# Kernel tuning notes

Measured on AMD Instinct MI355X. Metric: run time of the kernel, lower is better.

## Reference

```python
import jax, jax.numpy as jnp
import numpy as np

EPS = 1e-3  # Keras BatchNormalization default epsilon


def _bn(x, gamma, beta, mean, var):
    # inference-mode batchnorm over channel axis (last)
    inv = gamma * jax.lax.rsqrt(var + EPS)
    return x * inv + (beta - mean * inv)


def setup_inputs() -> dict:
    key = jax.random.key(0)
    ks = jax.random.split(key, 12)
    B, H, W, Cin = 8, 128, 128, 256
    F = 128  # f_g == f_l
    inp = {
        "input_g": jax.random.normal(ks[0], (B, H, W, Cin), jnp.float32),
        "input_x": jax.random.normal(ks[1], (B, H, W, Cin), jnp.float32),
        # w_g branch: 1x1 conv (channel GEMM) + BN
        "Wg": jax.random.normal(ks[2], (Cin, F), jnp.float32) * 0.05,
        "bg": jnp.zeros((F,), jnp.float32),
        "gamma_g": jax.random.uniform(ks[3], (F,), jnp.float32, 0.5, 1.5),
        "beta_g": jax.random.normal(ks[4], (F,), jnp.float32) * 0.1,
        "mean_g": jax.random.normal(ks[5], (F,), jnp.float32) * 0.1,
        "var_g": jax.random.uniform(ks[6], (F,), jnp.float32, 0.5, 1.5),
        # w_x branch
        "Wx": jax.random.normal(ks[7], (Cin, F), jnp.float32) * 0.05,
        "bx": jnp.zeros((F,), jnp.float32),
        "gamma_x": jax.random.uniform(ks[8], (F,), jnp.float32, 0.5, 1.5),
        "beta_x": jax.random.normal(ks[9], (F,), jnp.float32) * 0.1,
        "mean_x": jax.random.normal(ks[10], (F,), jnp.float32) * 0.1,
        "var_x": jax.random.uniform(ks[11], (F,), jnp.float32, 0.5, 1.5),
        # psi: F -> 1 conv + BN + sigmoid
        "Wp": jax.random.normal(jax.random.fold_in(key, 100), (F, 1), jnp.float32) * 0.05,
        "bp": jnp.zeros((1,), jnp.float32),
        "gamma_p": jnp.ones((1,), jnp.float32),
        "beta_p": jnp.zeros((1,), jnp.float32),
        "mean_p": jnp.zeros((1,), jnp.float32),
        "var_p": jnp.ones((1,), jnp.float32),
    }
    return inp


def reference(input_g, input_x, Wg, bg, gamma_g, beta_g, mean_g, var_g,
              Wx, bx, gamma_x, beta_x, mean_x, var_x,
              Wp, bp, gamma_p, beta_p, mean_p, var_p):
    # 1x1 convs are channel contractions: bhwc,cf->bhwf
    g = _bn(jnp.einsum('bhwc,cf->bhwf', input_g, Wg) + bg,
            gamma_g, beta_g, mean_g, var_g)
    x = _bn(jnp.einsum('bhwc,cf->bhwf', input_x, Wx) + bx,
            gamma_x, beta_x, mean_x, var_x)
    s = jax.nn.relu(g + x)                                 # [B,H,W,F]
    psi = jax.nn.sigmoid(_bn(jnp.einsum('bhwf,fo->bhwo', s, Wp) + bp,
                             gamma_p, beta_p, mean_p, var_p))  # [B,H,W,1]
    return x * psi
```

## Files before the change

### kernel.cpp

```cpp
#include <hip/hip_runtime.h>
#include <hip/hip_bf16.h>
#include <math.h>


typedef __bf16 bf16x8 __attribute__((ext_vector_type(8)));
typedef float f32x4 __attribute__((ext_vector_type(4)));

__device__ __forceinline__ unsigned short f2bf(float f) {
  union { float f; unsigned u; } v; v.f = f;
  unsigned r = (v.u + 0x7fffu + ((v.u >> 16) & 1u)) >> 16;
  return (unsigned short)r;
}

__device__ __forceinline__ bf16x8 cvt8(float4 a, float4 b) {
  bf16x8 r;
  r[0]=(__bf16)a.x; r[1]=(__bf16)a.y; r[2]=(__bf16)a.z; r[3]=(__bf16)a.w;
  r[4]=(__bf16)b.x; r[5]=(__bf16)b.y; r[6]=(__bf16)b.z; r[7]=(__bf16)b.w;
  return r;
}

__global__ __launch_bounds__(256) void fold_weights(
    const float* __restrict__ Wg, const float* __restrict__ bg,
    const float* __restrict__ gg, const float* __restrict__ beg,
    const float* __restrict__ mg, const float* __restrict__ vg,
    const float* __restrict__ Wx, const float* __restrict__ bx,
    const float* __restrict__ gx, const float* __restrict__ bex,
    const float* __restrict__ mx, const float* __restrict__ vx,
    const float* __restrict__ Wp, const float* __restrict__ bp,
    const float* __restrict__ gp, const float* __restrict__ bep,
    const float* __restrict__ mp, const float* __restrict__ vp,
    unsigned short* __restrict__ Bfg, unsigned short* __restrict__ Bfx,
    float* __restrict__ cg, float* __restrict__ cx,
    float* __restrict__ wps, float* __restrict__ cps) {
  int idx = blockIdx.x * 256 + threadIdx.x;
  int c = idx >> 7;
  int f = idx & 127;
  float ivg = gg[f] * rsqrtf(vg[f] + 1e-3f);
  float ivx = gx[f] * rsqrtf(vx[f] + 1e-3f);
  int ftile = f >> 4;
  int ksg = c >> 5;
  int lane = (((c >> 3) & 3) << 4) | (f & 15);
  int slot = c & 7;
  int off = ((ftile * 8 + ksg) * 64 + lane) * 8 + slot;
  Bfg[off] = f2bf(Wg[c * 128 + f] * ivg);
  Bfx[off] = f2bf(Wx[c * 128 + f] * ivx);
  if (idx < 128) {
    float ivg2 = gg[idx] * rsqrtf(vg[idx] + 1e-3f);
    float ivx2 = gx[idx] * rsqrtf(vx[idx] + 1e-3f);
    cg[idx] = bg[idx] * ivg2 + beg[idx] - mg[idx] * ivg2;
    cx[idx] = bx[idx] * ivx2 + bex[idx] - mx[idx] * ivx2;
    float ip = gp[0] * rsqrtf(vp[0] + 1e-3f);
    wps[idx] = Wp[idx] * ip;
    if (idx == 0) cps[0] = bp[0] * ip + bep[0] - mp[0] * ip;
  }
}

__global__ __launch_bounds__(512, 4) void attn_gate_main(
    const float* __restrict__ ing, const float* __restrict__ inx,
    const unsigned short* __restrict__ Wfg, const unsigned short* __restrict__ Wfx,
    const float* __restrict__ cgp, const float* __restrict__ cxp,
    const float* __restrict__ wpp, const float* __restrict__ cpp,
    float* __restrict__ out) {
  __shared__ __align__(16) short pixT[2][2][4096];
  __shared__ __align__(16) float xT[2][2048];
  __shared__ __align__(16) float psum[2][16][8];

  const int tid = threadIdx.x;
  const int lane = tid & 63;
  const int wid = tid >> 6;
  const int l15 = lane & 15, l4 = lane >> 4;

  bf16x8 wfg[8], wfx[8];
  #pragma unroll
  for (int ksg = 0; ksg < 8; ++ksg) {
    const int off = ((wid * 8 + ksg) * 64 + lane) * 8;
    wfg[ksg] = *reinterpret_cast<const bf16x8*>(Wfg + off);
    wfx[ksg] = *reinterpret_cast<const bf16x8*>(Wfx + off);
  }
  const int fb = wid * 16 + l4 * 4;
  const f32x4 cgv = *reinterpret_cast<const f32x4*>(cgp + fb);
  const f32x4 cxv = *reinterpret_cast<const f32x4*>(cxp + fb);
  const f32x4 wpv = *reinterpret_cast<const f32x4*>(wpp + fb);
  const float cpsv = cpp[0];

  const int spx = tid >> 5;
  const int sk = tid & 31;
  const int swoff = (spx << 9) | ((sk ^ ((spx & 7) << 2)) << 4);
  const long tile0 = (long)blockIdx.x * 8;
  const float* gsrc = ing + (tile0 * 16 + spx) * 256 + sk * 8;
  const float* xsrc = inx + (tile0 * 16 + spx) * 256 + sk * 8;

  {
    float4 a0 = *reinterpret_cast<const float4*>(gsrc);
    float4 a1 = *reinterpret_cast<const float4*>(gsrc + 4);
    float4 b0 = *reinterpret_cast<const float4*>(xsrc);
    float4 b1 = *reinterpret_cast<const float4*>(xsrc + 4);
    *reinterpret_cast<bf16x8*>((char*)&pixT[0][0][0] + swoff) = cvt8(a0, a1);
    *reinterpret_cast<bf16x8*>((char*)&pixT[0][1][0] + swoff) = cvt8(b0, b1);
  }
  __syncthreads();

  #pragma unroll 2
  for (int t = 0; t < 8; ++t) {
    const int buf = t & 1;
    float4 sg0, sg1, sx0, sx1;
    if (t < 7) {
      const float* g_ = gsrc + (t + 1) * 4096;
      const float* x_ = xsrc + (t + 1) * 4096;
      sg0 = *reinterpret_cast<const float4*>(g_);
      sg1 = *reinterpret_cast<const float4*>(g_ + 4);
      sx0 = *reinterpret_cast<const float4*>(x_);
      sx1 = *reinterpret_cast<const float4*>(x_ + 4);
    }

    f32x4 accg = {0.f, 0.f, 0.f, 0.f}, accx = {0.f, 0.f, 0.f, 0.f};
    #pragma unroll
    for (int ksg = 0; ksg < 8; ++ksg) {
      const int ra = (l15 << 9) | ((((ksg << 2) | l4) ^ ((l15 & 7) << 2)) << 4);
      bf16x8 pg = *reinterpret_cast<const bf16x8*>((const char*)&pixT[buf][0][0] + ra);
      bf16x8 px = *reinterpret_cast<const bf16x8*>((const char*)&pixT[buf][1][0] + ra);
      accg = __builtin_amdgcn_mfma_f32_16x16x32_bf16(wfg[ksg], pg, accg, 0, 0, 0);
      accx = __builtin_amdgcn_mfma_f32_16x16x32_bf16(wfx[ksg], px, accx, 0, 0, 0);
    }

    f32x4 xv;
    float part = 0.f;
    #pragma unroll
    for (int reg = 0; reg < 4; ++reg) {
      float gv = accg[reg] + cgv[reg];
      xv[reg] = accx[reg] + cxv[reg];
      float s = gv + xv[reg];
      s = s > 0.f ? s : 0.f;
      part += s * wpv[reg];
    }
    part += __shfl_xor(part, 16);
    part += __shfl_xor(part, 32);
    if (lane < 16) psum[buf][lane][wid] = part;
    const int xoff = (l15 << 9) | ((((wid << 2) | l4) ^ ((l15 & 7) << 2)) << 4);
    *reinterpret_cast<f32x4*>((char*)&xT[buf][0] + xoff) = xv;

    if (t < 7) {
      *reinterpret_cast<bf16x8*>((char*)&pixT[buf ^ 1][0][0] + swoff) = cvt8(sg0, sg1);
      *reinterpret_cast<bf16x8*>((char*)&pixT[buf ^ 1][1][0] + swoff) = cvt8(sx0, sx1);
    }
    __syncthreads();

    {
      const f32x4 pa = *reinterpret_cast<const f32x4*>(&psum[buf][spx][0]);
      const f32x4 pb = *reinterpret_cast<const f32x4*>(&psum[buf][spx][4]);
      const float z = pa[0] + pa[1] + pa[2] + pa[3]
                    + pb[0] + pb[1] + pb[2] + pb[3] + cpsv;
      const float psi = 1.f / (1.f + __expf(-z));
      f32x4 xr = *reinterpret_cast<const f32x4*>((const char*)&xT[buf][0] + swoff);
      xr[0] *= psi; xr[1] *= psi; xr[2] *= psi; xr[3] *= psi;
      *reinterpret_cast<f32x4*>(out + ((tile0 + t) * 16 + spx) * 128 + sk * 4) = xr;
    }
  }
}

extern "C" void kernel_launch(void* const* d_in, const int* in_sizes, int n_in,
                              void* d_out, int out_size, void* d_ws, size_t ws_size,
                              hipStream_t stream) {
  const float* ing = (const float*)d_in[0];
  const float* inx = (const float*)d_in[1];
  char* ws = (char*)d_ws;
  unsigned short* Bfg = (unsigned short*)ws;
  unsigned short* Bfx = (unsigned short*)(ws + 65536);
  float* cg  = (float*)(ws + 131072);
  float* cx  = (float*)(ws + 131584);
  float* wps = (float*)(ws + 132096);
  float* cps = (float*)(ws + 132608);

  fold_weights<<<128, 256, 0, stream>>>(
      (const float*)d_in[2],  (const float*)d_in[3],  (const float*)d_in[4],
      (const float*)d_in[5],  (const float*)d_in[6],  (const float*)d_in[7],
      (const float*)d_in[8],  (const float*)d_in[9],  (const float*)d_in[10],
      (const float*)d_in[11], (const float*)d_in[12], (const float*)d_in[13],
      (const float*)d_in[14], (const float*)d_in[15], (const float*)d_in[16],
      (const float*)d_in[17], (const float*)d_in[18], (const float*)d_in[19],
      Bfg, Bfx, cg, cx, wps, cps);

  const int npix = in_sizes[0] / 256;
  const int ntiles = npix / 16;
  attn_gate_main<<<ntiles / 8, 512, 0, stream>>>(
      ing, inx, Bfg, Bfx, cg, cx, wps, cps, (float*)d_out);
}
```

Measured before the change: 83.38 us.

## Write output directly from MFMA accumulators, drop xT LDS staging, retune swizzle

The x-branch result is no longer staged through shared memory for a coalesced store. Each lane now rescales its own accumulator values by psi and writes them straight to global memory. psum is transposed and padded so that each lane reads its pixel's partials across the 8 waves. The LDS swizzle XOR pattern is also changed, and launch bounds ask for 8 blocks per CU. This cuts LDS traffic and footprint, at the cost of global stores that are less contiguous (16-byte chunks spread over 16 pixel rows per wave) and tighter register pressure.

```diff
diff --git a/kernel.cpp b/kernel.cpp
--- a/kernel.cpp
+++ b/kernel.cpp
@@ -55,15 +55,14 @@
   }
 }
 
-__global__ __launch_bounds__(512, 4) void attn_gate_main(
+__global__ __launch_bounds__(512, 8) void attn_gate_main(
     const float* __restrict__ ing, const float* __restrict__ inx,
     const unsigned short* __restrict__ Wfg, const unsigned short* __restrict__ Wfx,
     const float* __restrict__ cgp, const float* __restrict__ cxp,
     const float* __restrict__ wpp, const float* __restrict__ cpp,
     float* __restrict__ out) {
   __shared__ __align__(16) short pixT[2][2][4096];
-  __shared__ __align__(16) float xT[2][2048];
-  __shared__ __align__(16) float psum[2][16][8];
+  __shared__ float psum[2][8][17];
 
   const int tid = threadIdx.x;
   const int lane = tid & 63;
@@ -85,7 +84,7 @@
 
   const int spx = tid >> 5;
   const int sk = tid & 31;
-  const int swoff = (spx << 9) | ((sk ^ ((spx & 7) << 2)) << 4);
+  const int swoff = (spx << 9) | ((sk ^ (spx & 7)) << 4);
   const long tile0 = (long)blockIdx.x * 8;
   const float* gsrc = ing + (tile0 * 16 + spx) * 256 + sk * 8;
   const float* xsrc = inx + (tile0 * 16 + spx) * 256 + sk * 8;
@@ -116,28 +115,25 @@
     f32x4 accg = {0.f, 0.f, 0.f, 0.f}, accx = {0.f, 0.f, 0.f, 0.f};
     #pragma unroll
     for (int ksg = 0; ksg < 8; ++ksg) {
-      const int ra = (l15 << 9) | ((((ksg << 2) | l4) ^ ((l15 & 7) << 2)) << 4);
+      const int ra = (l15 << 9) | ((((ksg << 2) | l4) ^ (l15 & 7)) << 4);
       bf16x8 pg = *reinterpret_cast<const bf16x8*>((const char*)&pixT[buf][0][0] + ra);
       bf16x8 px = *reinterpret_cast<const bf16x8*>((const char*)&pixT[buf][1][0] + ra);
       accg = __builtin_amdgcn_mfma_f32_16x16x32_bf16(wfg[ksg], pg, accg, 0, 0, 0);
       accx = __builtin_amdgcn_mfma_f32_16x16x32_bf16(wfx[ksg], px, accx, 0, 0, 0);
     }
 
-    f32x4 xv;
     float part = 0.f;
     #pragma unroll
     for (int reg = 0; reg < 4; ++reg) {
       float gv = accg[reg] + cgv[reg];
-      xv[reg] = accx[reg] + cxv[reg];
-      float s = gv + xv[reg];
+      float xv = accx[reg] + cxv[reg];
+      float s = gv + xv;
       s = s > 0.f ? s : 0.f;
       part += s * wpv[reg];
     }
     part += __shfl_xor(part, 16);
     part += __shfl_xor(part, 32);
-    if (lane < 16) psum[buf][lane][wid] = part;
-    const int xoff = (l15 << 9) | ((((wid << 2) | l4) ^ ((l15 & 7) << 2)) << 4);
-    *reinterpret_cast<f32x4*>((char*)&xT[buf][0] + xoff) = xv;
+    if (lane < 16) psum[buf][wid][lane] = part;
 
     if (t < 7) {
       *reinterpret_cast<bf16x8*>((char*)&pixT[buf ^ 1][0][0] + swoff) = cvt8(sg0, sg1);
@@ -146,14 +142,14 @@
     __syncthreads();
 
     {
-      const f32x4 pa = *reinterpret_cast<const f32x4*>(&psum[buf][spx][0]);
-      const f32x4 pb = *reinterpret_cast<const f32x4*>(&psum[buf][spx][4]);
-      const float z = pa[0] + pa[1] + pa[2] + pa[3]
-                    + pb[0] + pb[1] + pb[2] + pb[3] + cpsv;
+      float z = cpsv;
+      #pragma unroll
+      for (int w = 0; w < 8; ++w) z += psum[buf][w][l15];
       const float psi = 1.f / (1.f + __expf(-z));
-      f32x4 xr = *reinterpret_cast<const f32x4*>((const char*)&xT[buf][0] + swoff);
-      xr[0] *= psi; xr[1] *= psi; xr[2] *= psi; xr[3] *= psi;
-      *reinterpret_cast<f32x4*>(out + ((tile0 + t) * 16 + spx) * 128 + sk * 4) = xr;
+      f32x4 xr;
+      #pragma unroll
+      for (int reg = 0; reg < 4; ++reg) xr[reg] = (accx[reg] + cxv[reg]) * psi;
+      *reinterpret_cast<f32x4*>(out + ((tile0 + t) * 16 + l15) * 128 + fb) = xr;
     }
   }
 }
```

Result: slower. 239.5 us (+187.3%).
